# Kernel optimization log

Hardware: AMD Instinct MI355X
Metric: run time of the kernel (lower is better)

## Reference

```python
import jax, jax.numpy as jnp
import numpy as np

B, S, HID = 1, 2048, 2048
H, KVH, D, VD = 32, 8, 128, 128
R = 64  # rope_dim = head_dim * partial_rotary_factor, rounded down to even
N_REP = H // KVH
SCALE = D ** -0.5
NEG = -1e9


def _rotate_half(x):
    half = x.shape[-1] // 2
    return jnp.concatenate([-x[..., half:], x[..., :half]], axis=-1)


def setup_inputs() -> dict:
    key = jax.random.key(0)
    ks = jax.random.split(key, 8)
    hidden_states = jax.random.normal(ks[0], (B, S, HID), dtype=jnp.float32)
    # RoPE angles: standard inverse-frequency positional embedding of width R
    inv_freq = 1.0 / (10000.0 ** (np.arange(0, R, 2, dtype=np.float32) / R))
    pos = np.arange(S, dtype=np.float32)
    freqs = np.outer(pos, inv_freq)                       # [S, R/2]
    emb = np.concatenate([freqs, freqs], axis=-1)         # [S, R]
    cos = jnp.asarray(np.cos(emb))[None].repeat(B, axis=0)  # [B, S, R]
    sin = jnp.asarray(np.sin(emb))[None].repeat(B, axis=0)
    # additive causal mask [B, 1, S, S]
    causal = jnp.triu(jnp.full((S, S), NEG, dtype=jnp.float32), k=1)
    attention_mask = jnp.broadcast_to(causal[None, None], (B, 1, S, S))
    std = 0.02
    Wq = jax.random.normal(ks[1], (H * D, HID), dtype=jnp.float32) * std
    Wk = jax.random.normal(ks[2], (KVH * D, HID), dtype=jnp.float32) * std
    Wv = jax.random.normal(ks[3], (KVH * VD, HID), dtype=jnp.float32) * std
    Wo = jax.random.normal(ks[4], (HID, H * VD), dtype=jnp.float32) * std
    sink_bias = jax.random.normal(ks[5], (H,), dtype=jnp.float32) * 0.5
    return {"hidden_states": hidden_states, "cos": cos, "sin": sin,
            "attention_mask": attention_mask, "Wq": Wq, "Wk": Wk, "Wv": Wv,
            "Wo": Wo, "sink_bias": sink_bias}


def reference(hidden_states, cos, sin, attention_mask, Wq, Wk, Wv, Wo, sink_bias):
    b, s, _ = hidden_states.shape
    # projections -> [B, heads, S, dim]
    q = (hidden_states @ Wq.T).reshape(b, s, H, D).transpose(0, 2, 1, 3)
    k = (hidden_states @ Wk.T).reshape(b, s, KVH, D).transpose(0, 2, 1, 3)
    v = (hidden_states @ Wv.T).reshape(b, s, KVH, VD).transpose(0, 2, 1, 3)
    # partial RoPE on first R dims
    c = cos[:, None, :, :]  # [B,1,S,R]
    si = sin[:, None, :, :]
    q_r, q_n = q[..., :R], q[..., R:]
    k_r, k_n = k[..., :R], k[..., R:]
    q = jnp.concatenate([q_r * c + _rotate_half(q_r) * si, q_n], axis=-1)
    k = jnp.concatenate([k_r * c + _rotate_half(k_r) * si, k_n], axis=-1)
    # GQA: repeat kv heads
    k_rep = jnp.repeat(k, N_REP, axis=1)
    v_rep = jnp.repeat(v, N_REP, axis=1)
    scores = jnp.einsum('bhqd,bhkd->bhqk', q, k_rep) * SCALE + attention_mask
    # extra attention-sink logit column per head
    sinks = jnp.broadcast_to(sink_bias.reshape(1, H, 1, 1), (b, H, s, 1))
    aw = jnp.concatenate([scores, sinks], axis=-1)            # [B,H,S,S+1]
    probs = jax.nn.softmax(aw, axis=-1)[..., :-1]             # drop sink column
    out = jnp.einsum('bhqk,bhkd->bhqd', probs, v_rep)
    out = out.transpose(0, 2, 1, 3).reshape(b, s, H * VD)
    return out @ Wo.T
```

## Files before the change

kernel.cpp:

```cpp
#include <hip/hip_runtime.h>

typedef unsigned short u16;
typedef unsigned int   u32;
typedef __bf16  bf16x8 __attribute__((ext_vector_type(8)));
typedef float   f32x4  __attribute__((ext_vector_type(4)));
typedef u16     u16x4  __attribute__((ext_vector_type(4)));
typedef u16     u16x8  __attribute__((ext_vector_type(8)));

#define S_LEN 2048
#define NH 32
#define NKVH 8
#define HD 128
#define QKVST 6144
#define AOST  4096
#define ATT_SCALE 0.08838834764831845f
#define LOG2E 1.4426950408889634f
#define QSC2 (ATT_SCALE * LOG2E)
#define RESCALE_THR2 11.5f

__device__ __forceinline__ u16 f2bf(float f){
  u32 u = __builtin_bit_cast(u32, f);
  u += 0x7FFFu + ((u >> 16) & 1u);
  return (u16)(u >> 16);
}
__device__ __forceinline__ float bf2f(u16 h){
  u32 u = ((u32)h) << 16;
  return __builtin_bit_cast(float, u);
}
__device__ __forceinline__ void gload_lds16(const u16* g, u16* l){
  __builtin_amdgcn_global_load_lds(
      (const __attribute__((address_space(1))) void*)g,
      (__attribute__((address_space(3))) void*)l, 16, 0, 0);
}

__global__ void cvt_all_kernel(const f32x4* __restrict__ hs, const f32x4* __restrict__ wq,
                               const f32x4* __restrict__ wk, const f32x4* __restrict__ wv,
                               const f32x4* __restrict__ wo, u16x4* __restrict__ out){
  int i = blockIdx.x * 256 + threadIdx.x;
  const f32x4* src; int off;
  if      (i < 1048576){ src = hs; off = i; }
  else if (i < 3145728){ src = wq; off = i - 1048576; }
  else if (i < 3670016){ src = wk; off = i - 3145728; }
  else if (i < 4194304){ src = wv; off = i - 3670016; }
  else                 { src = wo; off = i - 4194304; }
  f32x4 v = src[off];
  u16x4 o;
  o[0] = f2bf(v[0]); o[1] = f2bf(v[1]); o[2] = f2bf(v[2]); o[3] = f2bf(v[3]);
  out[i] = o;
}

template<int OUT_BF16, int ROPE, int BN>
__global__ __launch_bounds__(256, 2)
void gemm_bt_kernel(const u16* __restrict__ X, const u16* __restrict__ W,
                    void* __restrict__ Cv, int M, int N, int K,
                    const float* __restrict__ cosv, const float* __restrict__ sinv){
  __shared__ __align__(16) u16 As[2][2][128 * 32];
  __shared__ __align__(16) u16 Bs[2][2][BN * 32];
  const int NJ = BN / 32;
  const int m0 = blockIdx.y * 128, n0 = blockIdx.x * BN;
  const int tid = threadIdx.x;
  const int wave = tid >> 6, lane = tid & 63;
  const int wm = wave >> 1, wn = wave & 1;
  const int g = lane >> 4, ln = lane & 15;
  const int r0 = tid >> 2;
  const int cc = (tid & 3) * 8;
  f32x4 acc[4][NJ] = {};
  const u16* xa0 = X + (size_t)(m0 + r0) * K + cc;
  const u16* xa1 = X + (size_t)(m0 + r0 + 64) * K + cc;
  const u16* wb0 = W + (size_t)(n0 + r0) * K + cc;
  const u16* wb1 = W + (size_t)(n0 + r0 + (BN == 128 ? 64 : 0)) * K + cc;

  auto stage = [&](int buf, int k0){
    #pragma unroll
    for (int s = 0; s < 2; s++){
      const int kc = k0 + s * 32;
      gload_lds16(xa0 + kc, &As[buf][s][tid * 8]);
      gload_lds16(xa1 + kc, &As[buf][s][2048 + tid * 8]);
      gload_lds16(wb0 + kc, &Bs[buf][s][tid * 8]);
      if (BN == 128) gload_lds16(wb1 + kc, &Bs[buf][s][2048 + tid * 8]);
    }
  };

  stage(0, 0);
  __syncthreads();
  int cur = 0;
  for (int k0 = 0; k0 < K; k0 += 64){
    if (k0 + 64 < K) stage(cur ^ 1, k0 + 64);
    #pragma unroll
    for (int s = 0; s < 2; s++){
      bf16x8 a[4], b[NJ];
      #pragma unroll
      for (int f = 0; f < 4; f++) a[f] = *(const bf16x8*)&As[cur][s][(wm * 64 + f * 16 + ln) * 32 + g * 8];
      #pragma unroll
      for (int f = 0; f < NJ; f++) b[f] = *(const bf16x8*)&Bs[cur][s][(wn * (BN / 2) + f * 16 + ln) * 32 + g * 8];
      __builtin_amdgcn_s_setprio(1);
      #pragma unroll
      for (int i = 0; i < 4; i++)
        #pragma unroll
        for (int j = 0; j < NJ; j++)
          acc[i][j] = __builtin_amdgcn_mfma_f32_16x16x32_bf16(a[i], b[j], acc[i][j], 0, 0, 0);
      __builtin_amdgcn_s_setprio(0);
    }
    __syncthreads();
    cur ^= 1;
  }
  if (ROPE && BN == 128){
    if (wn == 0 && n0 < 5120){
      #pragma unroll
      for (int i = 0; i < 4; i++)
        #pragma unroll
        for (int r = 0; r < 4; r++){
          const int row = m0 + wm * 64 + i * 16 + g * 4 + r;
          #pragma unroll
          for (int j = 0; j < 2; j++){
            const int d = j * 16 + ln;
            float c  = cosv[row * 64 + d];
            float sn = sinv[row * 64 + d];
            float x0 = acc[i][j][r], x1 = acc[i][j + 2][r];
            acc[i][j][r]     = x0 * c - x1 * sn;
            acc[i][j + 2][r] = x1 * c + x0 * sn;
          }
        }
    }
    if (n0 < 4096){
      #pragma unroll
      for (int i = 0; i < 4; i++)
        #pragma unroll
        for (int j = 0; j < 4; j++)
          #pragma unroll
          for (int r = 0; r < 4; r++) acc[i][j][r] *= QSC2;
    }
  }
  #pragma unroll
  for (int i = 0; i < 4; i++)
    #pragma unroll
    for (int j = 0; j < NJ; j++)
      #pragma unroll
      for (int r = 0; r < 4; r++){
        int row = m0 + wm * 64 + i * 16 + g * 4 + r;
        int col = n0 + wn * (BN / 2) + j * 16 + ln;
        if (OUT_BF16) ((u16*)Cv)[(size_t)row * N + col] = f2bf(acc[i][j][r]);
        else          ((float*)Cv)[(size_t)row * N + col] = acc[i][j][r];
      }
}

__global__ void vtrans_kernel(const u16* __restrict__ QKV, u16* __restrict__ VT){
  int idx = blockIdx.x * 256 + threadIdx.x;
  if (idx >= NKVH * HD * S_LEN) return;
  int s   = idx & (S_LEN - 1);
  int vd  = (idx >> 11) & (HD - 1);
  int kvh = idx >> 18;
  VT[idx] = QKV[(size_t)s * QKVST + 5120 + kvh * HD + vd];
}

__global__ __launch_bounds__(256, 2)
void attn_kernel(const u16* __restrict__ QKV, const u16* __restrict__ VT,
                 const float* __restrict__ sinkb, u16* __restrict__ AO){
  __shared__ __align__(16) u16 Ks[2][64 * 128];
  __shared__ __align__(16) u16 Vs[2][144 * 64];
  __shared__ __align__(16) u16 Ps[4][16 * 64];
  const int b   = blockIdx.x;
  const int kvh = b & 7;
  const int h   = kvh * 4 + ((b >> 3) & 3);
  const int qt  = 31 - (b >> 5);
  const int tid = threadIdx.x;
  const int w = tid >> 6, lane = tid & 63;
  const int g = lane >> 4, ln = lane & 15;
  const int q0 = qt * 64;
  const int qw = q0 + w * 16;

  const u16* Kbase = QKV + 4096 + kvh * HD;
  const u16* Vbase = VT + (size_t)kvh * HD * S_LEN;

  auto stage = [&](int buf, int kt){
    const int k0 = kt * 64;
    #pragma unroll
    for (int p = 0; p < 4; p++){
      int idx = p * 256 + tid;
      int r = idx >> 4, c16 = idx & 15;
      gload_lds16(Kbase + (size_t)(k0 + r) * QKVST + ((c16 ^ (r & 7)) * 8), &Ks[buf][idx * 8]);
    }
    #pragma unroll
    for (int p = 0; p < 4; p++){
      int idx = p * 256 + tid;
      int vd = idx >> 3, c8 = idx & 7;
      gload_lds16(Vbase + (size_t)vd * S_LEN + k0 + ((c8 ^ (vd & 7)) * 8), &Vs[buf][idx * 8]);
    }
  };

  for (int i = tid; i < 16 * 64; i += 256){
    u16 v = (i < 64) ? (u16)0x3F80 : (u16)0;
    Vs[0][128 * 64 + i] = v;
    Vs[1][128 * 64 + i] = v;
  }

  bf16x8 qf[4];
  const u16* qrow = QKV + (size_t)(qw + ln) * QKVST + h * HD;
  #pragma unroll
  for (int t = 0; t < 4; t++) qf[t] = *(const bf16x8*)(qrow + t * 32 + g * 8);

  const float sb2 = sinkb[h] * LOG2E;
  f32x4 O[9] = {};
  O[8][0] = O[8][1] = O[8][2] = O[8][3] = (ln == 0) ? 1.f : 0.f;
  float m_r[4];
  #pragma unroll
  for (int r = 0; r < 4; r++) m_r[r] = sb2;

  const int nkt = qt + 1;
  stage(0, 0);
  __syncthreads();
  int cur = 0;

  for (int kt = 0; kt < nkt; kt++){
    const int k0 = kt * 64;
    if (kt + 1 < nkt) stage(cur ^ 1, kt + 1);

    const u16* Kc = Ks[cur];
    f32x4 sc[4] = {};
    __builtin_amdgcn_s_setprio(1);
    #pragma unroll
    for (int f = 0; f < 4; f++){
      const int krow = f * 16 + ln;
      #pragma unroll
      for (int t = 0; t < 4; t++){
        bf16x8 kf = *(const bf16x8*)&Kc[krow * 128 + ((t * 32 + g * 8) ^ ((ln & 7) << 3))];
        sc[f] = __builtin_amdgcn_mfma_f32_16x16x32_bf16(qf[t], kf, sc[f], 0, 0, 0);
      }
    }
    __builtin_amdgcn_s_setprio(0);

    const bool diag = (kt == qt);
    if (diag){
      #pragma unroll
      for (int f = 0; f < 4; f++)
        #pragma unroll
        for (int r = 0; r < 4; r++)
          if (k0 + f * 16 + ln > qw + g * 4 + r) sc[f][r] = -1e30f;
    }
    float mx[4];
    #pragma unroll
    for (int r = 0; r < 4; r++){
      float t = fmaxf(fmaxf(sc[0][r], sc[1][r]), fmaxf(sc[2][r], sc[3][r]));
      #pragma unroll
      for (int d = 1; d < 16; d <<= 1) t = fmaxf(t, __shfl_xor(t, d));
      mx[r] = t;
    }
    int ok = (mx[0] <= m_r[0] + RESCALE_THR2) & (mx[1] <= m_r[1] + RESCALE_THR2)
           & (mx[2] <= m_r[2] + RESCALE_THR2) & (mx[3] <= m_r[3] + RESCALE_THR2);
    if (!__all(ok)){
      float sf_[4];
      #pragma unroll
      for (int r = 0; r < 4; r++){
        float mn = fmaxf(m_r[r], mx[r]);
        sf_[r] = exp2f(m_r[r] - mn);
        m_r[r] = mn;
      }
      #pragma unroll
      for (int fn = 0; fn < 9; fn++)
        #pragma unroll
        for (int r = 0; r < 4; r++) O[fn][r] *= sf_[r];
    }
    u16* Pw = Ps[w];
    #pragma unroll
    for (int r = 0; r < 4; r++){
      const int row = g * 4 + r;
      #pragma unroll
      for (int f = 0; f < 4; f++){
        float p = exp2f(sc[f][r] - m_r[r]);
        Pw[row * 64 + ((f * 16 + ln) ^ ((row & 7) << 3))] = f2bf(p);
      }
    }
    const u16* Vc = Vs[cur];
    bf16x8 pa0 = *(const bf16x8*)&Pw[ln * 64 + ((g * 8)      ^ ((ln & 7) << 3))];
    bf16x8 pa1 = *(const bf16x8*)&Pw[ln * 64 + ((32 + g * 8) ^ ((ln & 7) << 3))];
    __builtin_amdgcn_s_setprio(1);
    #pragma unroll
    for (int fn = 0; fn < 9; fn++){
      const int vr = fn * 16 + ln;
      bf16x8 v0 = *(const bf16x8*)&Vc[vr * 64 + ((g * 8)      ^ ((ln & 7) << 3))];
      bf16x8 v1 = *(const bf16x8*)&Vc[vr * 64 + ((32 + g * 8) ^ ((ln & 7) << 3))];
      O[fn] = __builtin_amdgcn_mfma_f32_16x16x32_bf16(pa0, v0, O[fn], 0, 0, 0);
      O[fn] = __builtin_amdgcn_mfma_f32_16x16x32_bf16(pa1, v1, O[fn], 0, 0, 0);
    }
    __builtin_amdgcn_s_setprio(0);

    __syncthreads();
    cur ^= 1;
  }
  #pragma unroll
  for (int r = 0; r < 4; r++){
    float l = __shfl(O[8][r], lane & 48);
    float osc = 1.f / l;
    #pragma unroll
    for (int fn = 0; fn < 8; fn++)
      AO[(size_t)(qw + g * 4 + r) * AOST + h * HD + fn * 16 + ln] = f2bf(O[fn][r] * osc);
  }
}

extern "C" void kernel_launch(void* const* d_in, const int* in_sizes, int n_in,
                              void* d_out, int out_size, void* d_ws, size_t ws_size,
                              hipStream_t stream){
  (void)in_sizes; (void)n_in; (void)out_size; (void)ws_size;
  const float* hs    = (const float*)d_in[0];
  const float* cosv  = (const float*)d_in[1];
  const float* sinv  = (const float*)d_in[2];
  const float* Wq    = (const float*)d_in[4];
  const float* Wk    = (const float*)d_in[5];
  const float* Wv    = (const float*)d_in[6];
  const float* Wo    = (const float*)d_in[7];
  const float* sinkb = (const float*)d_in[8];
  float* out = (float*)d_out;

  char* ws = (char*)d_ws;
  u16* XB    = (u16*)(ws);
  u16* WQKVB = (u16*)(ws + 8388608);
  u16* WOB   = (u16*)(ws + 33554432);
  u16* QKV   = (u16*)(ws + 50331648);
  u16* VT    = (u16*)(ws + 75497472);
  u16* AO    = (u16*)(ws + 79691776);

  cvt_all_kernel<<<24576, 256, 0, stream>>>((const f32x4*)hs, (const f32x4*)Wq,
                                            (const f32x4*)Wk, (const f32x4*)Wv,
                                            (const f32x4*)Wo, (u16x4*)ws);

  gemm_bt_kernel<1, 1, 128><<<dim3(48, 16), 256, 0, stream>>>(XB, WQKVB, QKV, 2048, 6144, 2048, cosv, sinv);

  vtrans_kernel<<<8192, 256, 0, stream>>>(QKV, VT);

  attn_kernel<<<dim3(1024), 256, 0, stream>>>(QKV, VT, sinkb, AO);

  gemm_bt_kernel<0, 0, 64><<<dim3(32, 16), 256, 0, stream>>>(AO, WOB, out, 2048, 2048, 4096, nullptr, nullptr);
}
```

Measured before the change: 242.7 us.

## Load K fragments directly from global into registers, drop K LDS staging

The attention kernel stops staging K tiles through shared memory. Each wave now loads its K MFMA fragments straight from global memory into registers at the start of every key tile. The row-sum ones-column is moved out of the V LDS buffer into a register constant, which shrinks shared memory use. With less LDS per block, launch bounds are raised to three blocks per CU. The cost is that every wave re-reads K from global/L2 with strided rows instead of sharing one LDS copy, and the load is no longer prefetched a tile ahead, so its latency may be exposed.

```diff
diff --git a/kernel.cpp b/kernel.cpp
--- a/kernel.cpp
+++ b/kernel.cpp
@@ -153,11 +153,10 @@
   VT[idx] = QKV[(size_t)s * QKVST + 5120 + kvh * HD + vd];
 }
 
-__global__ __launch_bounds__(256, 2)
+__global__ __launch_bounds__(256, 3)
 void attn_kernel(const u16* __restrict__ QKV, const u16* __restrict__ VT,
                  const float* __restrict__ sinkb, u16* __restrict__ AO){
-  __shared__ __align__(16) u16 Ks[2][64 * 128];
-  __shared__ __align__(16) u16 Vs[2][144 * 64];
+  __shared__ __align__(16) u16 Vs[2][128 * 64];
   __shared__ __align__(16) u16 Ps[4][16 * 64];
   const int b   = blockIdx.x;
   const int kvh = b & 7;
@@ -169,17 +168,11 @@
   const int q0 = qt * 64;
   const int qw = q0 + w * 16;
 
-  const u16* Kbase = QKV + 4096 + kvh * HD;
   const u16* Vbase = VT + (size_t)kvh * HD * S_LEN;
+  const u16* Kl = QKV + 4096 + kvh * HD + (size_t)ln * QKVST + g * 8;
 
   auto stage = [&](int buf, int kt){
     const int k0 = kt * 64;
-    #pragma unroll
-    for (int p = 0; p < 4; p++){
-      int idx = p * 256 + tid;
-      int r = idx >> 4, c16 = idx & 15;
-      gload_lds16(Kbase + (size_t)(k0 + r) * QKVST + ((c16 ^ (r & 7)) * 8), &Ks[buf][idx * 8]);
-    }
     #pragma unroll
     for (int p = 0; p < 4; p++){
       int idx = p * 256 + tid;
@@ -188,11 +181,10 @@
     }
   };
 
-  for (int i = tid; i < 16 * 64; i += 256){
-    u16 v = (i < 64) ? (u16)0x3F80 : (u16)0;
-    Vs[0][128 * 64 + i] = v;
-    Vs[1][128 * 64 + i] = v;
-  }
+  u16x8 ob;
+  #pragma unroll
+  for (int j = 0; j < 8; j++) ob[j] = (ln == 0) ? (u16)0x3F80 : (u16)0;
+  const bf16x8 onesf = __builtin_bit_cast(bf16x8, ob);
 
   bf16x8 qf[4];
   const u16* qrow = QKV + (size_t)(qw + ln) * QKVST + h * HD;
@@ -200,8 +192,9 @@
   for (int t = 0; t < 4; t++) qf[t] = *(const bf16x8*)(qrow + t * 32 + g * 8);
 
   const float sb2 = sinkb[h] * LOG2E;
-  f32x4 O[9] = {};
-  O[8][0] = O[8][1] = O[8][2] = O[8][3] = (ln == 0) ? 1.f : 0.f;
+  f32x4 O[8] = {};
+  f32x4 L;
+  L[0] = L[1] = L[2] = L[3] = (ln == 0) ? 1.f : 0.f;
   float m_r[4];
   #pragma unroll
   for (int r = 0; r < 4; r++) m_r[r] = sb2;
@@ -213,20 +206,23 @@
 
   for (int kt = 0; kt < nkt; kt++){
     const int k0 = kt * 64;
+
+    bf16x8 kbuf[4][4];
+    #pragma unroll
+    for (int f = 0; f < 4; f++)
+      #pragma unroll
+      for (int t = 0; t < 4; t++)
+        kbuf[f][t] = *(const bf16x8*)(Kl + (size_t)(k0 + f * 16) * QKVST + t * 32);
+
     if (kt + 1 < nkt) stage(cur ^ 1, kt + 1);
 
-    const u16* Kc = Ks[cur];
     f32x4 sc[4] = {};
     __builtin_amdgcn_s_setprio(1);
     #pragma unroll
-    for (int f = 0; f < 4; f++){
-      const int krow = f * 16 + ln;
-      #pragma unroll
-      for (int t = 0; t < 4; t++){
-        bf16x8 kf = *(const bf16x8*)&Kc[krow * 128 + ((t * 32 + g * 8) ^ ((ln & 7) << 3))];
-        sc[f] = __builtin_amdgcn_mfma_f32_16x16x32_bf16(qf[t], kf, sc[f], 0, 0, 0);
-      }
-    }
+    for (int f = 0; f < 4; f++)
+      #pragma unroll
+      for (int t = 0; t < 4; t++)
+        sc[f] = __builtin_amdgcn_mfma_f32_16x16x32_bf16(qf[t], kbuf[f][t], sc[f], 0, 0, 0);
     __builtin_amdgcn_s_setprio(0);
 
     const bool diag = (kt == qt);
@@ -256,9 +252,11 @@
         m_r[r] = mn;
       }
       #pragma unroll
-      for (int fn = 0; fn < 9; fn++)
+      for (int fn = 0; fn < 8; fn++)
         #pragma unroll
         for (int r = 0; r < 4; r++) O[fn][r] *= sf_[r];
+      #pragma unroll
+      for (int r = 0; r < 4; r++) L[r] *= sf_[r];
     }
     u16* Pw = Ps[w];
     #pragma unroll
@@ -275,13 +273,15 @@
     bf16x8 pa1 = *(const bf16x8*)&Pw[ln * 64 + ((32 + g * 8) ^ ((ln & 7) << 3))];
     __builtin_amdgcn_s_setprio(1);
     #pragma unroll
-    for (int fn = 0; fn < 9; fn++){
+    for (int fn = 0; fn < 8; fn++){
       const int vr = fn * 16 + ln;
       bf16x8 v0 = *(const bf16x8*)&Vc[vr * 64 + ((g * 8)      ^ ((ln & 7) << 3))];
       bf16x8 v1 = *(const bf16x8*)&Vc[vr * 64 + ((32 + g * 8) ^ ((ln & 7) << 3))];
       O[fn] = __builtin_amdgcn_mfma_f32_16x16x32_bf16(pa0, v0, O[fn], 0, 0, 0);
       O[fn] = __builtin_amdgcn_mfma_f32_16x16x32_bf16(pa1, v1, O[fn], 0, 0, 0);
     }
+    L = __builtin_amdgcn_mfma_f32_16x16x32_bf16(pa0, onesf, L, 0, 0, 0);
+    L = __builtin_amdgcn_mfma_f32_16x16x32_bf16(pa1, onesf, L, 0, 0, 0);
     __builtin_amdgcn_s_setprio(0);
 
     __syncthreads();
@@ -289,7 +289,7 @@
   }
   #pragma unroll
   for (int r = 0; r < 4; r++){
-    float l = __shfl(O[8][r], lane & 48);
+    float l = __shfl(L[r], lane & 48);
     float osc = 1.f / l;
     #pragma unroll
     for (int fn = 0; fn < 8; fn++)
```

Result: slower. 329.4 us (+35.7%).

## Rewrite attention with 32x32 MFMA, 128-row query tiles and register-resident P

Applied to the files above, without the earlier changes.

Restructures the attention kernel to use 32x32x16 bf16 MFMAs with each wave owning 32 query rows, giving 128-query tiles and half as many blocks. S is computed transposed so probabilities stay in registers: they are packed with v_cvt_pk_bf16_f32 and exchanged across lanes with v_permlane32_swap, which removes the LDS round-trip for P. The row sum is now accumulated in scalar registers instead of through an extra ones-column MFMA. Output is staged through LDS for coalesced 16-byte stores, and the tile order is remapped for causal load balance. The cost is larger per-wave register state and fewer blocks, and waves whose rows end early skip compute on some key tiles but still wait at every barrier.

```diff
diff --git a/kernel.cpp b/kernel.cpp
--- a/kernel.cpp
+++ b/kernel.cpp
@@ -4,8 +4,10 @@
 typedef unsigned int   u32;
 typedef __bf16  bf16x8 __attribute__((ext_vector_type(8)));
 typedef float   f32x4  __attribute__((ext_vector_type(4)));
+typedef float   f32x16 __attribute__((ext_vector_type(16)));
 typedef u16     u16x4  __attribute__((ext_vector_type(4)));
 typedef u16     u16x8  __attribute__((ext_vector_type(8)));
+typedef u32     u32x4  __attribute__((ext_vector_type(4)));
 
 #define S_LEN 2048
 #define NH 32
@@ -23,9 +25,10 @@
   u += 0x7FFFu + ((u >> 16) & 1u);
   return (u16)(u >> 16);
 }
-__device__ __forceinline__ float bf2f(u16 h){
-  u32 u = ((u32)h) << 16;
-  return __builtin_bit_cast(float, u);
+__device__ __forceinline__ u32 cvtpk(float lo, float hi){
+  u32 d;
+  asm("v_cvt_pk_bf16_f32 %0, %1, %2" : "=v"(d) : "v"(lo), "v"(hi));
+  return d;
 }
 __device__ __forceinline__ void gload_lds16(const u16* g, u16* l){
   __builtin_amdgcn_global_load_lds(
@@ -156,18 +159,19 @@
 __global__ __launch_bounds__(256, 2)
 void attn_kernel(const u16* __restrict__ QKV, const u16* __restrict__ VT,
                  const float* __restrict__ sinkb, u16* __restrict__ AO){
-  __shared__ __align__(16) u16 Ks[2][64 * 128];
-  __shared__ __align__(16) u16 Vs[2][144 * 64];
-  __shared__ __align__(16) u16 Ps[4][16 * 64];
-  const int b   = blockIdx.x;
-  const int kvh = b & 7;
-  const int h   = kvh * 4 + ((b >> 3) & 3);
-  const int qt  = 31 - (b >> 5);
-  const int tid = threadIdx.x;
-  const int w = tid >> 6, lane = tid & 63;
-  const int g = lane >> 4, ln = lane & 15;
-  const int q0 = qt * 64;
-  const int qw = q0 + w * 16;
+  __shared__ __align__(16) u16 Ks[2][32 * 256];
+  __shared__ __align__(16) u16 Vs[2][32 * 256];
+  const int b    = blockIdx.x;
+  const int kvh  = b & 7;
+  const int head = kvh * 4 + ((b >> 3) & 3);
+  const int slot = b >> 5;
+  const int qt   = (slot < 8) ? (15 - slot) : (slot - 8);
+  const int tid  = threadIdx.x;
+  const int w    = tid >> 6;
+  const int lane = tid & 63;
+  const int l31  = lane & 31, hi = lane >> 5;
+  const int q0   = qt * 128;
+  const int qw   = q0 + w * 32;
 
   const u16* Kbase = QKV + 4096 + kvh * HD;
   const u16* Vbase = VT + (size_t)kvh * HD * S_LEN;
@@ -177,36 +181,31 @@
     #pragma unroll
     for (int p = 0; p < 4; p++){
       int idx = p * 256 + tid;
-      int r = idx >> 4, c16 = idx & 15;
-      gload_lds16(Kbase + (size_t)(k0 + r) * QKVST + ((c16 ^ (r & 7)) * 8), &Ks[buf][idx * 8]);
+      int r = idx >> 5, c = idx & 31;
+      int cs = c ^ r;
+      int key = r * 2 + (cs >> 4), d8 = (cs & 15) * 8;
+      gload_lds16(Kbase + (size_t)(k0 + key) * QKVST + d8, &Ks[buf][idx * 8]);
     }
     #pragma unroll
     for (int p = 0; p < 4; p++){
       int idx = p * 256 + tid;
-      int vd = idx >> 3, c8 = idx & 7;
-      gload_lds16(Vbase + (size_t)vd * S_LEN + k0 + ((c8 ^ (vd & 7)) * 8), &Vs[buf][idx * 8]);
+      int r = idx >> 5, c = idx & 31;
+      int cs = c ^ r;
+      int vd = r * 4 + (cs >> 3), k8 = (cs & 7) * 8;
+      gload_lds16(Vbase + (size_t)vd * S_LEN + k0 + k8, &Vs[buf][idx * 8]);
     }
   };
 
-  for (int i = tid; i < 16 * 64; i += 256){
-    u16 v = (i < 64) ? (u16)0x3F80 : (u16)0;
-    Vs[0][128 * 64 + i] = v;
-    Vs[1][128 * 64 + i] = v;
-  }
-
-  bf16x8 qf[4];
-  const u16* qrow = QKV + (size_t)(qw + ln) * QKVST + h * HD;
+  bf16x8 qB[8];
+  const u16* qrow = QKV + (size_t)(qw + l31) * QKVST + head * HD;
   #pragma unroll
-  for (int t = 0; t < 4; t++) qf[t] = *(const bf16x8*)(qrow + t * 32 + g * 8);
-
-  const float sb2 = sinkb[h] * LOG2E;
-  f32x4 O[9] = {};
-  O[8][0] = O[8][1] = O[8][2] = O[8][3] = (ln == 0) ? 1.f : 0.f;
-  float m_r[4];
-  #pragma unroll
-  for (int r = 0; r < 4; r++) m_r[r] = sb2;
-
-  const int nkt = qt + 1;
+  for (int t = 0; t < 8; t++) qB[t] = *(const bf16x8*)(qrow + t * 16 + hi * 8);
+
+  float m  = sinkb[head] * LOG2E;
+  float Ll = (hi == 0) ? 1.f : 0.f;
+  f32x16 O[4] = {};
+
+  const int nkt = 2 * qt + 2;
   stage(0, 0);
   __syncthreads();
   int cur = 0;
@@ -215,85 +214,98 @@
     const int k0 = kt * 64;
     if (kt + 1 < nkt) stage(cur ^ 1, kt + 1);
 
-    const u16* Kc = Ks[cur];
-    f32x4 sc[4] = {};
-    __builtin_amdgcn_s_setprio(1);
-    #pragma unroll
-    for (int f = 0; f < 4; f++){
-      const int krow = f * 16 + ln;
-      #pragma unroll
-      for (int t = 0; t < 4; t++){
-        bf16x8 kf = *(const bf16x8*)&Kc[krow * 128 + ((t * 32 + g * 8) ^ ((ln & 7) << 3))];
-        sc[f] = __builtin_amdgcn_mfma_f32_16x16x32_bf16(qf[t], kf, sc[f], 0, 0, 0);
-      }
-    }
-    __builtin_amdgcn_s_setprio(0);
-
-    const bool diag = (kt == qt);
-    if (diag){
-      #pragma unroll
-      for (int f = 0; f < 4; f++)
-        #pragma unroll
-        for (int r = 0; r < 4; r++)
-          if (k0 + f * 16 + ln > qw + g * 4 + r) sc[f][r] = -1e30f;
-    }
-    float mx[4];
-    #pragma unroll
-    for (int r = 0; r < 4; r++){
-      float t = fmaxf(fmaxf(sc[0][r], sc[1][r]), fmaxf(sc[2][r], sc[3][r]));
-      #pragma unroll
-      for (int d = 1; d < 16; d <<= 1) t = fmaxf(t, __shfl_xor(t, d));
-      mx[r] = t;
-    }
-    int ok = (mx[0] <= m_r[0] + RESCALE_THR2) & (mx[1] <= m_r[1] + RESCALE_THR2)
-           & (mx[2] <= m_r[2] + RESCALE_THR2) & (mx[3] <= m_r[3] + RESCALE_THR2);
-    if (!__all(ok)){
-      float sf_[4];
-      #pragma unroll
-      for (int r = 0; r < 4; r++){
-        float mn = fmaxf(m_r[r], mx[r]);
-        sf_[r] = exp2f(m_r[r] - mn);
-        m_r[r] = mn;
-      }
-      #pragma unroll
-      for (int fn = 0; fn < 9; fn++)
-        #pragma unroll
-        for (int r = 0; r < 4; r++) O[fn][r] *= sf_[r];
-    }
-    u16* Pw = Ps[w];
-    #pragma unroll
-    for (int r = 0; r < 4; r++){
-      const int row = g * 4 + r;
-      #pragma unroll
-      for (int f = 0; f < 4; f++){
-        float p = exp2f(sc[f][r] - m_r[r]);
-        Pw[row * 64 + ((f * 16 + ln) ^ ((row & 7) << 3))] = f2bf(p);
-      }
-    }
-    const u16* Vc = Vs[cur];
-    bf16x8 pa0 = *(const bf16x8*)&Pw[ln * 64 + ((g * 8)      ^ ((ln & 7) << 3))];
-    bf16x8 pa1 = *(const bf16x8*)&Pw[ln * 64 + ((32 + g * 8) ^ ((ln & 7) << 3))];
-    __builtin_amdgcn_s_setprio(1);
-    #pragma unroll
-    for (int fn = 0; fn < 9; fn++){
-      const int vr = fn * 16 + ln;
-      bf16x8 v0 = *(const bf16x8*)&Vc[vr * 64 + ((g * 8)      ^ ((ln & 7) << 3))];
-      bf16x8 v1 = *(const bf16x8*)&Vc[vr * 64 + ((32 + g * 8) ^ ((ln & 7) << 3))];
-      O[fn] = __builtin_amdgcn_mfma_f32_16x16x32_bf16(pa0, v0, O[fn], 0, 0, 0);
-      O[fn] = __builtin_amdgcn_mfma_f32_16x16x32_bf16(pa1, v1, O[fn], 0, 0, 0);
-    }
-    __builtin_amdgcn_s_setprio(0);
-
+    if (k0 < qw + 32){
+      const u16* Kc = Ks[cur];
+      const u16* Vc = Vs[cur];
+      f32x16 sc0 = {}, sc1 = {};
+      const int krow0 = (l31 >> 1);
+      const int kc0   = ((l31 & 1) << 4) | hi;
+      __builtin_amdgcn_s_setprio(1);
+      #pragma unroll
+      for (int t = 0; t < 8; t++){
+        bf16x8 ka0 = *(const bf16x8*)&Kc[krow0 * 256 + ((kc0 + 2 * t) ^ krow0) * 8];
+        bf16x8 ka1 = *(const bf16x8*)&Kc[(16 + krow0) * 256 + ((kc0 + 2 * t) ^ (16 + krow0)) * 8];
+        sc0 = __builtin_amdgcn_mfma_f32_32x32x16_bf16(ka0, qB[t], sc0, 0, 0, 0);
+        sc1 = __builtin_amdgcn_mfma_f32_32x32x16_bf16(ka1, qB[t], sc1, 0, 0, 0);
+      }
+      __builtin_amdgcn_s_setprio(0);
+
+      if (k0 + 63 > qw){
+        const int qg = qw + l31;
+        #pragma unroll
+        for (int r = 0; r < 16; r++){
+          int keyr = k0 + (r & 3) + 8 * (r >> 2) + 4 * hi;
+          if (keyr      > qg) sc0[r] = -1e30f;
+          if (keyr + 32 > qg) sc1[r] = -1e30f;
+        }
+      }
+      float mx = sc0[0];
+      #pragma unroll
+      for (int r = 1; r < 16; r++) mx = fmaxf(mx, sc0[r]);
+      #pragma unroll
+      for (int r = 0; r < 16; r++) mx = fmaxf(mx, sc1[r]);
+      mx = fmaxf(mx, __shfl_xor(mx, 32));
+      if (!__all(mx <= m + RESCALE_THR2)){
+        float mn = fmaxf(m, mx);
+        float sf = exp2f(m - mn);
+        m = mn;
+        #pragma unroll
+        for (int n = 0; n < 4; n++)
+          #pragma unroll
+          for (int r = 0; r < 16; r++) O[n][r] *= sf;
+        Ll *= sf;
+      }
+      float p0[16], p1[16];
+      #pragma unroll
+      for (int r = 0; r < 16; r++){ p0[r] = exp2f(sc0[r] - m); Ll += p0[r]; }
+      #pragma unroll
+      for (int r = 0; r < 16; r++){ p1[r] = exp2f(sc1[r] - m); Ll += p1[r]; }
+
+      __builtin_amdgcn_s_setprio(1);
+      #pragma unroll
+      for (int c = 0; c < 4; c++){
+        const float* ps = (c & 2) ? p1 : p0;
+        const int bb = (c & 1) * 8;
+        u32 wa = cvtpk(ps[bb + 0], ps[bb + 1]);
+        u32 wb = cvtpk(ps[bb + 2], ps[bb + 3]);
+        u32 wc = cvtpk(ps[bb + 4], ps[bb + 5]);
+        u32 wd = cvtpk(ps[bb + 6], ps[bb + 7]);
+        asm("v_permlane32_swap_b32 %0, %1" : "+v"(wa), "+v"(wc));
+        asm("v_permlane32_swap_b32 %0, %1" : "+v"(wb), "+v"(wd));
+        u32x4 wv_; wv_[0] = wa; wv_[1] = wb; wv_[2] = wc; wv_[3] = wd;
+        bf16x8 pf = __builtin_bit_cast(bf16x8, wv_);
+        #pragma unroll
+        for (int n = 0; n < 4; n++){
+          const int vrow = n * 8 + (l31 >> 2);
+          const int vcc  = ((l31 & 3) << 3) | (c << 1) | hi;
+          bf16x8 va = *(const bf16x8*)&Vc[vrow * 256 + (vcc ^ vrow) * 8];
+          O[n] = __builtin_amdgcn_mfma_f32_32x32x16_bf16(va, pf, O[n], 0, 0, 0);
+        }
+      }
+      __builtin_amdgcn_s_setprio(0);
+    }
     __syncthreads();
     cur ^= 1;
   }
+
+  float l = Ll + __shfl_xor(Ll, 32);
+  float inv = 1.f / l;
+  u16* arena = &Ks[0][0];
   #pragma unroll
-  for (int r = 0; r < 4; r++){
-    float l = __shfl(O[8][r], lane & 48);
-    float osc = 1.f / l;
-    #pragma unroll
-    for (int fn = 0; fn < 8; fn++)
-      AO[(size_t)(qw + g * 4 + r) * AOST + h * HD + fn * 16 + ln] = f2bf(O[fn][r] * osc);
+  for (int n = 0; n < 4; n++)
+    #pragma unroll
+    for (int r = 0; r < 16; r++){
+      int vd = n * 32 + (r & 3) + 8 * (r >> 2) + 4 * hi;
+      int ch = (vd >> 3) ^ (l31 & 15);
+      arena[w * 4096 + l31 * 128 + ch * 8 + (vd & 7)] = f2bf(O[n][r] * inv);
+    }
+  __syncthreads();
+  #pragma unroll
+  for (int p = 0; p < 8; p++){
+    int idx = p * 256 + tid;
+    int row = idx >> 4, c = idx & 15;
+    u16x8 v = *(const u16x8*)&arena[row * 128 + ((c ^ (row & 15)) * 8)];
+    *(u16x8*)&AO[(size_t)(q0 + row) * AOST + head * HD + c * 8] = v;
   }
 }
 
@@ -327,7 +339,7 @@
 
   vtrans_kernel<<<8192, 256, 0, stream>>>(QKV, VT);
 
-  attn_kernel<<<dim3(1024), 256, 0, stream>>>(QKV, VT, sinkb, AO);
+  attn_kernel<<<dim3(512), 256, 0, stream>>>(QKV, VT, sinkb, AO);
 
   gemm_bt_kernel<0, 0, 64><<<dim3(32, 16), 256, 0, stream>>>(AO, WOB, out, 2048, 2048, 4096, nullptr, nullptr);
 }
```

Result: no change. 239.2 us (-1.4%).
